# Kernel tuning notes

Measured on AMD Instinct MI355X. Metric: run time of the kernel, lower is better.

## Reference

```python
import jax, jax.numpy as jnp
import numpy as np

WIRES = 4
LAYERS = 3
DIM = 2 ** WIRES  # 16-dim state vector, wire 0 = most significant bit (PennyLane convention)


def _cnot_perm(c, t):
    # CNOT is a basis permutation (its own inverse): new_amp[b] = old_amp[perm[b]]
    perm = np.arange(DIM)
    for b in range(DIM):
        if (b >> (WIRES - 1 - c)) & 1:
            perm[b] = b ^ (1 << (WIRES - 1 - t))
    return jnp.asarray(perm)

PERM01 = _cnot_perm(0, 1)
PERM23 = _cnot_perm(2, 3)


def _apply_ry(state, cq, sq, q):
    # state: (N, 16) real (RY and CNOT keep |0000> real). Split axis of qubit q.
    N = state.shape[0]
    st = state.reshape(N, 2 ** q, 2, 2 ** (WIRES - 1 - q))
    a0, a1 = st[:, :, 0, :], st[:, :, 1, :]
    cq = cq[:, None, None]
    sq = sq[:, None, None]
    new = jnp.stack([cq * a0 - sq * a1, sq * a0 + cq * a1], axis=2)
    return new.reshape(N, DIM)


def _simulate(angles):
    # angles: (N, 4) -> PauliZ expvals (N, 4)
    N = angles.shape[0]
    half = angles * 0.5
    c = jnp.cos(half)
    s = jnp.sin(half)
    state = jnp.zeros((N, DIM), angles.dtype).at[:, 0].set(1.0)

    def ry_layer(st):
        for q in range(WIRES):
            st = _apply_ry(st, c[:, q], s[:, q], q)
        return st

    state = ry_layer(state)  # initial encoding layer
    for _ in range(LAYERS):
        state = ry_layer(state)
        state = state[:, PERM01]  # CNOT(0,1)
        state = state[:, PERM23]  # CNOT(2,3)

    probs = state * state
    zs = []
    for q in range(WIRES):
        p = probs.reshape(N, 2 ** q, 2, 2 ** (WIRES - 1 - q))
        zs.append(p[:, :, 0, :].sum((1, 2)) - p[:, :, 1, :].sum((1, 2)))
    return jnp.stack(zs, axis=1)


def setup_inputs() -> dict:
    key = jax.random.key(0)
    k1, k2 = jax.random.split(key)
    B = 8192
    x = jax.random.normal(k1, (B, 1, 28, 28), dtype=jnp.float32)
    W = jax.random.normal(k2, (784, 1), dtype=jnp.float32) * 0.02
    b = jnp.zeros((1,), dtype=jnp.float32)
    return {"x": x, "W": W, "b": b}


def reference(x, W, b):
    B = x.shape[0]
    img = x[:, 0]  # (B, 28, 28)
    # non-overlapping 2x2 patches in row-major (r, c) order, each flattened row-major
    patches = img.reshape(B, 14, 2, 14, 2).transpose(0, 1, 3, 2, 4).reshape(B, 196, 4)
    angles = jnp.clip(patches, -1.0, 1.0) * jnp.pi
    feats = _simulate(angles.reshape(B * 196, 4)).reshape(B, 196 * 4)
    return jax.nn.sigmoid(feats @ W + b)
```

## Files before the change

### kernel.cpp

```cpp
#include <hip/hip_runtime.h>
#include <math.h>


__device__ __forceinline__ float reg2(float t0, float t1, float w0, float w1) {
    const float u0 = fminf(fmaxf(t0, -1.0f), 1.0f);
    const float u1 = fminf(fmaxf(t1, -1.0f), 1.0f);
    const float s0 = __builtin_amdgcn_sinf(u0 * 0.25f);
    const float c0 = __builtin_amdgcn_cosf(u0 * 0.25f);
    const float s1 = __builtin_amdgcn_sinf(u1 * 0.25f);
    const float c1 = __builtin_amdgcn_cosf(u1 * 0.25f);
    const float c20 = fmaf(-2.0f * s0, s0, 1.0f);
    const float s20 = (s0 + s0) * c0;
    const float c21 = fmaf(-2.0f * s1, s1, 1.0f);
    const float s21 = (s1 + s1) * c1;

    float A0 = c20 * c21, A1 = c20 * s21, A2 = s20 * s21, A3 = s20 * c21;

    #pragma unroll
    for (int l = 0; l < 2; ++l) {
        const float n0 = c0 * A0 - s0 * A2;
        const float n2 = s0 * A0 + c0 * A2;
        const float n1 = c0 * A1 - s0 * A3;
        const float n3 = s0 * A1 + c0 * A3;
        A0 = c1 * n0 - s1 * n1;
        A1 = s1 * n0 + c1 * n1;
        A2 = c1 * n2 - s1 * n3;
        A3 = s1 * n2 + c1 * n3;
        const float tt = A2; A2 = A3; A3 = tt;
    }

    const float p0 = A0 * A0, p1 = A1 * A1, p2 = A2 * A2, p3 = A3 * A3;
    return (p0 - p3) * (w0 + w1) + (p1 - p2) * (w0 - w1);
}

__device__ __forceinline__ float sim_patch(float t0, float t1, float t2, float t3,
                                           const float4 w) {
    return reg2(t0, t1, w.x, w.y) + reg2(t2, t3, w.z, w.w);
}

__global__ __launch_bounds__(128) void fraud_kernel(
    const float* __restrict__ x,
    const float* __restrict__ W,
    const float* __restrict__ bias,
    float* __restrict__ out)
{
    const int tid = threadIdx.x;
    const unsigned img = blockIdx.x;

    const unsigned pp = (tid < 98) ? (unsigned)tid : 0u;
    const unsigned i  = pp / 7u;
    const unsigned jj = pp - i * 7u;

    const float* rowp = x + (size_t)img * 784 + (2u * i) * 28 + 4u * jj;
    const float4 ra = *reinterpret_cast<const float4*>(rowp);
    const float4 rb = *reinterpret_cast<const float4*>(rowp + 28);
    const float4 wA = *reinterpret_cast<const float4*>(W + 8u * pp);
    const float4 wB = *reinterpret_cast<const float4*>(W + 8u * pp + 4);

    float partial = sim_patch(ra.x, ra.y, rb.x, rb.y, wA)
                  + sim_patch(ra.z, ra.w, rb.z, rb.w, wB);
    if (tid >= 98) partial = 0.0f;

    #pragma unroll
    for (int off = 32; off > 0; off >>= 1)
        partial += __shfl_xor(partial, off, 64);

    __shared__ float red[2];
    if ((tid & 63) == 0) red[tid >> 6] = partial;
    __syncthreads();

    if (tid == 0) {
        const float v = red[0] + red[1] + bias[0];
        out[img] = 1.0f / (1.0f + __expf(-v));
    }
}

extern "C" void kernel_launch(void* const* d_in, const int* in_sizes, int n_in,
                              void* d_out, int out_size, void* d_ws, size_t ws_size,
                              hipStream_t stream) {
    const float* x    = (const float*)d_in[0];
    const float* W    = (const float*)d_in[1];
    const float* bias = (const float*)d_in[2];
    float* out = (float*)d_out;

    const int B = out_size;
    fraud_kernel<<<dim3(B), dim3(128), 0, stream>>>(x, W, bias, out);
}
```

Baseline: 15.44 us.

## Map one image per wavefront and drop shared-memory block reduction

New measurement: 16.72 us. +8.3%, slower.

```diff
diff --git a/kernel.cpp b/kernel.cpp
--- a/kernel.cpp
+++ b/kernel.cpp
@@ -33,46 +33,52 @@
     return (p0 - p3) * (w0 + w1) + (p1 - p2) * (w0 - w1);
 }
 
-__device__ __forceinline__ float sim_patch(float t0, float t1, float t2, float t3,
-                                           const float4 w) {
-    return reg2(t0, t1, w.x, w.y) + reg2(t2, t3, w.z, w.w);
+__device__ __forceinline__ float hpair(const float4 ra, const float4 rb,
+                                       const float4 wA, const float4 wB) {
+    return reg2(ra.x, ra.y, wA.x, wA.y) + reg2(rb.x, rb.y, wA.z, wA.w)
+         + reg2(ra.z, ra.w, wB.x, wB.y) + reg2(rb.z, rb.w, wB.z, wB.w);
 }
 
-__global__ __launch_bounds__(128) void fraud_kernel(
+__global__ __launch_bounds__(256) void fraud_kernel(
     const float* __restrict__ x,
     const float* __restrict__ W,
     const float* __restrict__ bias,
     float* __restrict__ out)
 {
-    const int tid = threadIdx.x;
-    const unsigned img = blockIdx.x;
+    const int tid  = threadIdx.x;
+    const int lane = tid & 63;
+    const unsigned img = blockIdx.x * 4u + (unsigned)(tid >> 6);
 
-    const unsigned pp = (tid < 98) ? (unsigned)tid : 0u;
-    const unsigned i  = pp / 7u;
-    const unsigned jj = pp - i * 7u;
+    const float* ximg = x + (size_t)img * 784;
 
-    const float* rowp = x + (size_t)img * 784 + (2u * i) * 28 + 4u * jj;
-    const float4 ra = *reinterpret_cast<const float4*>(rowp);
-    const float4 rb = *reinterpret_cast<const float4*>(rowp + 28);
-    const float4 wA = *reinterpret_cast<const float4*>(W + 8u * pp);
-    const float4 wB = *reinterpret_cast<const float4*>(W + 8u * pp + 4);
+    const unsigned i1  = (unsigned)lane / 7u;
+    const unsigned jj1 = (unsigned)lane - i1 * 7u;
+    const float* p1 = ximg + (2u * i1) * 28 + 4u * jj1;
+    const float4 ra1 = *reinterpret_cast<const float4*>(p1);
+    const float4 rb1 = *reinterpret_cast<const float4*>(p1 + 28);
+    const float4 wA1 = *reinterpret_cast<const float4*>(W + 8u * (unsigned)lane);
+    const float4 wB1 = *reinterpret_cast<const float4*>(W + 8u * (unsigned)lane + 4);
 
-    float partial = sim_patch(ra.x, ra.y, rb.x, rb.y, wA)
-                  + sim_patch(ra.z, ra.w, rb.z, rb.w, wB);
-    if (tid >= 98) partial = 0.0f;
+    float partial = hpair(ra1, rb1, wA1, wB1);
+
+    if (lane < 34) {
+        const unsigned pp  = 64u + (unsigned)lane;
+        const unsigned i2  = pp / 7u;
+        const unsigned jj2 = pp - i2 * 7u;
+        const float* p2 = ximg + (2u * i2) * 28 + 4u * jj2;
+        const float4 ra2 = *reinterpret_cast<const float4*>(p2);
+        const float4 rb2 = *reinterpret_cast<const float4*>(p2 + 28);
+        const float4 wA2 = *reinterpret_cast<const float4*>(W + 8u * pp);
+        const float4 wB2 = *reinterpret_cast<const float4*>(W + 8u * pp + 4);
+        partial += hpair(ra2, rb2, wA2, wB2);
+    }
 
     #pragma unroll
     for (int off = 32; off > 0; off >>= 1)
         partial += __shfl_xor(partial, off, 64);
 
-    __shared__ float red[2];
-    if ((tid & 63) == 0) red[tid >> 6] = partial;
-    __syncthreads();
-
-    if (tid == 0) {
-        const float v = red[0] + red[1] + bias[0];
-        out[img] = 1.0f / (1.0f + __expf(-v));
-    }
+    if (lane == 0)
+        out[img] = 1.0f / (1.0f + __expf(-(partial + bias[0])));
 }
 
 extern "C" void kernel_launch(void* const* d_in, const int* in_sizes, int n_in,
@@ -84,5 +90,5 @@
     float* out = (float*)d_out;
 
     const int B = out_size;
-    fraud_kernel<<<dim3(B), dim3(128), 0, stream>>>(x, W, bias, out);
+    fraud_kernel<<<dim3(B / 4), dim3(256), 0, stream>>>(x, W, bias, out);
 }
```
